# Performance work log

Hardware: AMD Instinct MI355X
Metric: run time of the kernel (lower is better)

The kernel has to match this reference:

```python
import jax, jax.numpy as jnp
import numpy as np

N = 128   # system size (number of sequential RNN steps)
B = 8192  # batch of samples
H = 128   # hidden units per layer (units=[128,128])
D = 2     # input_dim (spin up/down one-hot)


def setup_inputs() -> dict:
    key = jax.random.key(0)
    ks = jax.random.split(key, 11)
    s = 1.0 / np.sqrt(H)  # torch nn.RNNCell/Linear default U(-1/sqrt(H), 1/sqrt(H))
    bits = jax.random.randint(ks[0], (N, B), 0, D)
    samples = jax.nn.one_hot(bits, D, dtype=jnp.float32)  # (N, B, D) one-hot spins
    u = lambda k, shp: jax.random.uniform(k, shp, jnp.float32, -s, s)
    return {
        "samples": samples,
        "W_ih0": u(ks[1], (H, D)), "b_ih0": u(ks[2], (H,)),
        "W_hh0": u(ks[3], (H, H)), "b_hh0": u(ks[4], (H,)),
        "W_ih1": u(ks[5], (H, H)), "b_ih1": u(ks[6], (H,)),
        "W_hh1": u(ks[7], (H, H)), "b_hh1": u(ks[8], (H,)),
        "W_dense": u(ks[9], (D, H)), "b_dense": u(ks[10], (D,)),
    }


def reference(samples, W_ih0, b_ih0, W_hh0, b_hh0,
              W_ih1, b_ih1, W_hh1, b_hh1, W_dense, b_dense):
    # Faithful jax port of RNN_wavefunction.log_prob:
    # p_t = <softmax(dense(h1_t)), s_t>; returns sum_t log p_t with shape (1, B).
    # For one-hot s_t, log(sum(prob*s_t)) == sum(s_t * log_softmax(logits)) (stable form).
    Bsz = samples.shape[1]
    # input at step t is the sampled spin from step t-1; zeros at t=0
    inputs = jnp.concatenate(
        [jnp.zeros((1, Bsz, D), samples.dtype), samples[:-1]], axis=0)
    h0 = jnp.zeros((Bsz, H), samples.dtype)
    h1 = jnp.zeros((Bsz, H), samples.dtype)

    def step(carry, xs):
        h0, h1 = carry
        x_t, s_t = xs  # x_t: (B, D) prev spin one-hot, s_t: (B, D) current spin
        # nn.RNNCell: h' = tanh(x W_ih^T + b_ih + h W_hh^T + b_hh)
        h0 = jnp.tanh(x_t @ W_ih0.T + b_ih0 + h0 @ W_hh0.T + b_hh0)
        h1 = jnp.tanh(h0 @ W_ih1.T + b_ih1 + h1 @ W_hh1.T + b_hh1)
        logits = h1 @ W_dense.T + b_dense           # (B, 2)
        logp = jax.nn.log_softmax(logits, axis=-1)
        lp_t = jnp.sum(logp * s_t, axis=-1)          # (B,) = log p(s_t)
        return (h0, h1), lp_t

    _, lps = jax.lax.scan(step, (h0, h1), (inputs, samples))  # lps: (N, B)
    return jnp.sum(lps, axis=0, keepdims=True)  # (1, B), matches torch keepdim=True
```

## Files before the change

### kernel.cpp

```cpp
#include <hip/hip_runtime.h>
#include <hip/hip_bf16.h>


#define NSTEP 128
#define BTOT  8192
#define HID   128
#define MB    16
#define NBLK  (BTOT / MB)
#define NTHR  512

typedef __attribute__((ext_vector_type(8))) short bf16x8;
typedef __attribute__((ext_vector_type(4))) float f32x4;
typedef __attribute__((ext_vector_type(2))) float f32x2;
typedef __attribute__((ext_vector_type(2))) unsigned uint32x2;

__device__ __forceinline__ short f2bf(float v) {
    unsigned u = __builtin_bit_cast(unsigned, v);
    u += 0x7FFFu + ((u >> 16) & 1u);
    return (short)(u >> 16);
}
__device__ __forceinline__ unsigned cvt2bf(float a, float b) {
    __hip_bfloat162 h2 = __float22bfloat162_rn(make_float2(a, b));
    unsigned u; __builtin_memcpy(&u, &h2, sizeof(u));
    return u;
}
__device__ __forceinline__ f32x2 tanh2(f32x2 x) {
    f32x2 z = x * 2.885390081777927f;
    float e0 = __builtin_exp2f(z.x);
    float e1 = __builtin_exp2f(z.y);
    f32x2 d = {e0 + 1.0f, e1 + 1.0f};
    float r = __builtin_amdgcn_rcpf(d.x * d.y);
    f32x2 inv = {r * d.y, r * d.x};
    return inv * -2.0f + 1.0f;
}

__global__ __launch_bounds__(NTHR, 4) void rnn_wf_kernel(
    const float* __restrict__ samples,
    const float* __restrict__ Wih0,
    const float* __restrict__ bih0,
    const float* __restrict__ Whh0,
    const float* __restrict__ bhh0,
    const float* __restrict__ Wih1,
    const float* __restrict__ bih1,
    const float* __restrict__ Whh1,
    const float* __restrict__ bhh1,
    const float* __restrict__ Wd,
    const float* __restrict__ bd,
    float* __restrict__ out)
{
    __shared__ short sH0[2][MB * HID];
    __shared__ short sH1[2][MB * HID];
    __shared__ unsigned sMask[NSTEP];
    __shared__ float sLd[NSTEP * 17];
    __shared__ __attribute__((aligned(16))) float sBias[4 * HID];
    __shared__ __attribute__((aligned(16))) short sFwd[4 * 64 * 8];

    const int tid  = threadIdx.x;
    const int b0   = blockIdx.x * MB;
    const int w    = tid >> 6;
    const int lane = tid & 63;
    const int q    = lane >> 4;
    const int c    = lane & 15;

    if (tid < NSTEP) {
        unsigned msk = 0;
        #pragma unroll
        for (int m = 0; m < MB; ++m) {
            float e1 = samples[((size_t)tid * BTOT + b0 + m) * 2 + 1];
            if (e1 > 0.5f) msk |= (1u << m);
        }
        sMask[tid] = msk;
    }
    if (tid >= NSTEP && tid < NSTEP + HID) {
        const int n = tid - NSTEP;
        const float bb = bih0[n] + bhh0[n];
        sBias[n]       = bb + Wih0[n * 2 + 0];
        sBias[128 + n] = bb + Wih0[n * 2 + 1];
        sBias[256 + n] = bih1[n] + bhh1[n];
        sBias[384 + n] = bb;
    }
    if (tid >= 256 && tid < 512) {
        const int t2 = tid - 256;
        const int kb = t2 >> 6, l = t2 & 63, cc = l & 15, qq = l >> 4;
        bf16x8 v;
        #pragma unroll
        for (int j = 0; j < 8; ++j)
            v[j] = (cc < 2) ? f2bf(Wd[cc * HID + kb * 32 + qq * 8 + j]) : (short)0;
        *reinterpret_cast<bf16x8*>(&sFwd[(kb * 64 + l) * 8]) = v;
    }

    bf16x8 fhh0[4], fih1[4], fhh1[4];
    {
        const int nn = w * 16 + c;
        #pragma unroll
        for (int kb = 0; kb < 4; ++kb) {
            const int off = nn * HID + kb * 32 + q * 8;
            bf16x8 v0, v1, v2;
            #pragma unroll
            for (int j = 0; j < 8; ++j) {
                v0[j] = f2bf(Whh0[off + j]);
                v1[j] = f2bf(Wih1[off + j]);
                v2[j] = f2bf(Whh1[off + j]);
            }
            fhh0[kb] = v0; fih1[kb] = v1; fhh1[kb] = v2;
        }
    }
    const float bd0 = bd[0], bd1 = bd[1];

    int ra[4];
    #pragma unroll
    for (int kb = 0; kb < 4; ++kb)
        ra[kb] = c * HID + (((kb * 4 + q) ^ c) << 3);
    const int wa = c * HID + (((2 * w + (q >> 1)) ^ c) << 3) + ((q & 1) << 2);
    const int ib = w * 16 + q * 4;

    bool bmPrev = false;

    auto storeL = [&](short* buf, const f32x4& a) {
        f32x2 t0 = tanh2((f32x2){a[0], a[1]});
        f32x2 t1 = tanh2((f32x2){a[2], a[3]});
        uint32x2 v = {cvt2bf(t0.x, t0.y), cvt2bf(t1.x, t1.y)};
        *reinterpret_cast<uint32x2*>(&buf[wa]) = v;
    };

    __syncthreads();

    storeL(sH0[1], *reinterpret_cast<const f32x4*>(&sBias[384 + ib]));
    __syncthreads();

    {
        const bool bmIn = (sMask[0] >> c) & 1u;
        const float* bp = bmIn ? (sBias + 128) : sBias;
        f32x4 a0 = *reinterpret_cast<const f32x4*>(&bp[ib]);
        f32x4 a1 = *reinterpret_cast<const f32x4*>(&sBias[256 + ib]);
        #pragma unroll
        for (int kb = 0; kb < 4; ++kb) {
            bf16x8 f0 = *reinterpret_cast<const bf16x8*>(&sH0[1][ra[kb]]);
            a0 = __builtin_amdgcn_mfma_f32_16x16x32_bf16(fhh0[kb], f0, a0, 0, 0, 0);
            a1 = __builtin_amdgcn_mfma_f32_16x16x32_bf16(fih1[kb], f0, a1, 0, 0, 0);
        }
        storeL(sH0[0], a0);
        storeL(sH1[0], a1);
        bmPrev = bmIn;
        __syncthreads();
    }

    auto stepMain = [&](int i, const short* r0, const short* r1,
                        short* w0b, short* w1b) {
        const bool bmIn = (sMask[i - 1] >> c) & 1u;
        const float* bp = bmIn ? (sBias + 128) : sBias;
        f32x4 a0 = *reinterpret_cast<const f32x4*>(&bp[ib]);
        f32x4 a1 = *reinterpret_cast<const f32x4*>(&sBias[256 + ib]);
        bf16x8 f0[4], f1[4];
        #pragma unroll
        for (int kb = 0; kb < 4; ++kb) {
            f0[kb] = *reinterpret_cast<const bf16x8*>(&r0[ra[kb]]);
            f1[kb] = *reinterpret_cast<const bf16x8*>(&r1[ra[kb]]);
        }
        #pragma unroll
        for (int kb = 0; kb < 4; ++kb) {
            a0 = __builtin_amdgcn_mfma_f32_16x16x32_bf16(fhh0[kb], f0[kb], a0, 0, 0, 0);
            a1 = __builtin_amdgcn_mfma_f32_16x16x32_bf16(fhh1[kb], f1[kb], a1, 0, 0, 0);
        }
        #pragma unroll
        for (int kb = 0; kb < 4; ++kb)
            a1 = __builtin_amdgcn_mfma_f32_16x16x32_bf16(fih1[kb], f0[kb], a1, 0, 0, 0);
        if (w == (i & 7)) {
            f32x4 aL = {bd0, bd1, 0.f, 0.f};
            #pragma unroll
            for (int kb = 0; kb < 4; ++kb) {
                bf16x8 fw = *reinterpret_cast<const bf16x8*>(&sFwd[(kb * 64 + lane) * 8]);
                aL = __builtin_amdgcn_mfma_f32_16x16x32_bf16(fw, f1[kb], aL, 0, 0, 0);
            }
            if (q == 0)
                sLd[(i - 2) * 17 + c] = bmPrev ? (aL[0] - aL[1]) : (aL[1] - aL[0]);
        }
        bmPrev = bmIn;
        storeL(w0b, a0);
        storeL(w1b, a1);
        __syncthreads();
    };

    for (int i = 2; i < NSTEP; i += 2) {
        stepMain(i,     sH0[0], sH1[0], sH0[1], sH1[1]);
        stepMain(i + 1, sH0[1], sH1[1], sH0[0], sH1[0]);
    }

    {
        f32x4 a1 = *reinterpret_cast<const f32x4*>(&sBias[256 + ib]);
        bf16x8 f0[4], f1[4];
        #pragma unroll
        for (int kb = 0; kb < 4; ++kb) {
            f0[kb] = *reinterpret_cast<const bf16x8*>(&sH0[0][ra[kb]]);
            f1[kb] = *reinterpret_cast<const bf16x8*>(&sH1[0][ra[kb]]);
        }
        #pragma unroll
        for (int kb = 0; kb < 4; ++kb)
            a1 = __builtin_amdgcn_mfma_f32_16x16x32_bf16(fhh1[kb], f1[kb], a1, 0, 0, 0);
        #pragma unroll
        for (int kb = 0; kb < 4; ++kb)
            a1 = __builtin_amdgcn_mfma_f32_16x16x32_bf16(fih1[kb], f0[kb], a1, 0, 0, 0);
        if (w == 0) {
            f32x4 aL = {bd0, bd1, 0.f, 0.f};
            #pragma unroll
            for (int kb = 0; kb < 4; ++kb) {
                bf16x8 fw = *reinterpret_cast<const bf16x8*>(&sFwd[(kb * 64 + lane) * 8]);
                aL = __builtin_amdgcn_mfma_f32_16x16x32_bf16(fw, f1[kb], aL, 0, 0, 0);
            }
            if (q == 0)
                sLd[126 * 17 + c] = bmPrev ? (aL[0] - aL[1]) : (aL[1] - aL[0]);
        }
        storeL(sH1[1], a1);
        __syncthreads();
    }
    if (w == 1) {
        f32x4 aL = {bd0, bd1, 0.f, 0.f};
        #pragma unroll
        for (int kb = 0; kb < 4; ++kb) {
            bf16x8 f1 = *reinterpret_cast<const bf16x8*>(&sH1[1][ra[kb]]);
            bf16x8 fw = *reinterpret_cast<const bf16x8*>(&sFwd[(kb * 64 + lane) * 8]);
            aL = __builtin_amdgcn_mfma_f32_16x16x32_bf16(fw, f1, aL, 0, 0, 0);
        }
        if (q == 0) {
            const bool bit = (sMask[NSTEP - 1] >> c) & 1u;
            sLd[127 * 17 + c] = bit ? (aL[0] - aL[1]) : (aL[1] - aL[0]);
        }
    }
    __syncthreads();

    if (tid < 256) {
        const int s = tid >> 4;
        const int k = tid & 15;
        float acc = 0.0f;
        #pragma unroll
        for (int j = 0; j < 8; ++j) {
            const float x = sLd[(j * 16 + k) * 17 + s];
            const float ed = __builtin_exp2f(x * 1.4426950408889634f);
            acc -= 0.6931471805599453f * __builtin_log2f(1.0f + ed);
        }
        #pragma unroll
        for (int off = 1; off < 16; off <<= 1)
            acc += __shfl_xor(acc, off, 64);
        if (k == 0)
            out[b0 + s] = acc;
    }
}

extern "C" void kernel_launch(void* const* d_in, const int* in_sizes, int n_in,
                              void* d_out, int out_size, void* d_ws, size_t ws_size,
                              hipStream_t stream) {
    rnn_wf_kernel<<<NBLK, NTHR, 0, stream>>>(
        (const float*)d_in[0],
        (const float*)d_in[1],
        (const float*)d_in[2],
        (const float*)d_in[3],
        (const float*)d_in[4],
        (const float*)d_in[5],
        (const float*)d_in[6],
        (const float*)d_in[7],
        (const float*)d_in[8],
        (const float*)d_in[9],
        (const float*)d_in[10],
        (float*)d_out);
}
```

Before: 239.3 us.

## Halve block to 4 waves, each computing two output tiles with register-held biases

Each block now runs 256 threads (4 waves) instead of 512, and each wave computes two 16-row tiles of the hidden output per step. The per-step load of LDS data for hidden-state fragments is shared across both tiles. Biases and the dense weight fragments move from shared memory into registers. tanh now uses two reciprocals in place of one shared reciprocal. The change aims to cut redundant LDS fragment reads and make barriers cheaper, at the cost of roughly doubled VGPR use per thread (launch bounds 2) and longer serial MFMA chains per wave.

```diff
diff --git a/kernel.cpp b/kernel.cpp
--- a/kernel.cpp
+++ b/kernel.cpp
@@ -7,7 +7,7 @@
 #define HID   128
 #define MB    16
 #define NBLK  (BTOT / MB)
-#define NTHR  512
+#define NTHR  256
 
 typedef __attribute__((ext_vector_type(8))) short bf16x8;
 typedef __attribute__((ext_vector_type(4))) float f32x4;
@@ -26,15 +26,13 @@
 }
 __device__ __forceinline__ f32x2 tanh2(f32x2 x) {
     f32x2 z = x * 2.885390081777927f;
-    float e0 = __builtin_exp2f(z.x);
-    float e1 = __builtin_exp2f(z.y);
-    f32x2 d = {e0 + 1.0f, e1 + 1.0f};
-    float r = __builtin_amdgcn_rcpf(d.x * d.y);
-    f32x2 inv = {r * d.y, r * d.x};
-    return inv * -2.0f + 1.0f;
-}
-
-__global__ __launch_bounds__(NTHR, 4) void rnn_wf_kernel(
+    float r0 = __builtin_amdgcn_rcpf(__builtin_exp2f(z.x) + 1.0f);
+    float r1 = __builtin_amdgcn_rcpf(__builtin_exp2f(z.y) + 1.0f);
+    f32x2 r = {r0, r1};
+    return r * -2.0f + 1.0f;
+}
+
+__global__ __launch_bounds__(NTHR, 2) void rnn_wf_kernel(
     const float* __restrict__ samples,
     const float* __restrict__ Wih0,
     const float* __restrict__ bih0,
@@ -52,8 +50,6 @@
     __shared__ short sH1[2][MB * HID];
     __shared__ unsigned sMask[NSTEP];
     __shared__ float sLd[NSTEP * 17];
-    __shared__ __attribute__((aligned(16))) float sBias[4 * HID];
-    __shared__ __attribute__((aligned(16))) short sFwd[4 * 64 * 8];
 
     const int tid  = threadIdx.x;
     const int b0   = blockIdx.x * MB;
@@ -71,39 +67,53 @@
         }
         sMask[tid] = msk;
     }
-    if (tid >= NSTEP && tid < NSTEP + HID) {
-        const int n = tid - NSTEP;
-        const float bb = bih0[n] + bhh0[n];
-        sBias[n]       = bb + Wih0[n * 2 + 0];
-        sBias[128 + n] = bb + Wih0[n * 2 + 1];
-        sBias[256 + n] = bih1[n] + bhh1[n];
-        sBias[384 + n] = bb;
-    }
-    if (tid >= 256 && tid < 512) {
-        const int t2 = tid - 256;
-        const int kb = t2 >> 6, l = t2 & 63, cc = l & 15, qq = l >> 4;
-        bf16x8 v;
-        #pragma unroll
-        for (int j = 0; j < 8; ++j)
-            v[j] = (cc < 2) ? f2bf(Wd[cc * HID + kb * 32 + qq * 8 + j]) : (short)0;
-        *reinterpret_cast<bf16x8*>(&sFwd[(kb * 64 + l) * 8]) = v;
-    }
-
-    bf16x8 fhh0[4], fih1[4], fhh1[4];
-    {
-        const int nn = w * 16 + c;
-        #pragma unroll
-        for (int kb = 0; kb < 4; ++kb) {
-            const int off = nn * HID + kb * 32 + q * 8;
-            bf16x8 v0, v1, v2;
-            #pragma unroll
-            for (int j = 0; j < 8; ++j) {
-                v0[j] = f2bf(Whh0[off + j]);
-                v1[j] = f2bf(Wih1[off + j]);
-                v2[j] = f2bf(Whh1[off + j]);
+
+    bf16x8 fhh0[2][4], fih1[2][4], fhh1[2][4], fw[4];
+    {
+        auto ldf = [](const float* p) {
+            f32x4 l0 = *reinterpret_cast<const f32x4*>(p);
+            f32x4 l1 = *reinterpret_cast<const f32x4*>(p + 4);
+            bf16x8 v;
+            v[0]=f2bf(l0[0]); v[1]=f2bf(l0[1]); v[2]=f2bf(l0[2]); v[3]=f2bf(l0[3]);
+            v[4]=f2bf(l1[0]); v[5]=f2bf(l1[1]); v[6]=f2bf(l1[2]); v[7]=f2bf(l1[3]);
+            return v;
+        };
+        #pragma unroll
+        for (int t = 0; t < 2; ++t) {
+            const int nn = w * 32 + t * 16 + c;
+            #pragma unroll
+            for (int kb = 0; kb < 4; ++kb) {
+                const int off = nn * HID + kb * 32 + q * 8;
+                fhh0[t][kb] = ldf(Whh0 + off);
+                fih1[t][kb] = ldf(Wih1 + off);
+                fhh1[t][kb] = ldf(Whh1 + off);
             }
-            fhh0[kb] = v0; fih1[kb] = v1; fhh1[kb] = v2;
-        }
+        }
+        #pragma unroll
+        for (int kb = 0; kb < 4; ++kb) {
+            bf16x8 v;
+            #pragma unroll
+            for (int j = 0; j < 8; ++j)
+                v[j] = (c < 2) ? f2bf(Wd[c * HID + kb * 32 + q * 8 + j]) : (short)0;
+            fw[kb] = v;
+        }
+    }
+
+    f32x4 bWA[2], bWB[2], bB1[2], bP[2];
+    #pragma unroll
+    for (int t = 0; t < 2; ++t) {
+        const int n0 = w * 32 + t * 16 + q * 4;
+        f32x4 vi = *reinterpret_cast<const f32x4*>(&bih0[n0]);
+        f32x4 vh = *reinterpret_cast<const f32x4*>(&bhh0[n0]);
+        f32x4 bb = vi + vh;
+        f32x4 wA = *reinterpret_cast<const f32x4*>(&Wih0[n0 * 2]);
+        f32x4 wB = *reinterpret_cast<const f32x4*>(&Wih0[n0 * 2 + 4]);
+        bP[t]  = bb;
+        bWA[t] = bb + (f32x4){wA[0], wA[2], wB[0], wB[2]};
+        bWB[t] = bb + (f32x4){wA[1], wA[3], wB[1], wB[3]};
+        f32x4 v1 = *reinterpret_cast<const f32x4*>(&bih1[n0]);
+        f32x4 v2 = *reinterpret_cast<const f32x4*>(&bhh1[n0]);
+        bB1[t] = v1 + v2;
     }
     const float bd0 = bd[0], bd1 = bd[1];
 
@@ -111,36 +121,45 @@
     #pragma unroll
     for (int kb = 0; kb < 4; ++kb)
         ra[kb] = c * HID + (((kb * 4 + q) ^ c) << 3);
-    const int wa = c * HID + (((2 * w + (q >> 1)) ^ c) << 3) + ((q & 1) << 2);
-    const int ib = w * 16 + q * 4;
+    int wa[2];
+    #pragma unroll
+    for (int t = 0; t < 2; ++t)
+        wa[t] = c * HID + (((4 * w + 2 * t + (q >> 1)) ^ c) << 3) + ((q & 1) << 2);
 
     bool bmPrev = false;
 
-    auto storeL = [&](short* buf, const f32x4& a) {
+    auto storeT = [&](short* buf, int t, const f32x4& a) {
         f32x2 t0 = tanh2((f32x2){a[0], a[1]});
         f32x2 t1 = tanh2((f32x2){a[2], a[3]});
         uint32x2 v = {cvt2bf(t0.x, t0.y), cvt2bf(t1.x, t1.y)};
-        *reinterpret_cast<uint32x2*>(&buf[wa]) = v;
+        *reinterpret_cast<uint32x2*>(&buf[wa[t]]) = v;
     };
 
     __syncthreads();
 
-    storeL(sH0[1], *reinterpret_cast<const f32x4*>(&sBias[384 + ib]));
+    storeT(sH0[1], 0, bP[0]);
+    storeT(sH0[1], 1, bP[1]);
     __syncthreads();
 
     {
         const bool bmIn = (sMask[0] >> c) & 1u;
-        const float* bp = bmIn ? (sBias + 128) : sBias;
-        f32x4 a0 = *reinterpret_cast<const f32x4*>(&bp[ib]);
-        f32x4 a1 = *reinterpret_cast<const f32x4*>(&sBias[256 + ib]);
-        #pragma unroll
-        for (int kb = 0; kb < 4; ++kb) {
-            bf16x8 f0 = *reinterpret_cast<const bf16x8*>(&sH0[1][ra[kb]]);
-            a0 = __builtin_amdgcn_mfma_f32_16x16x32_bf16(fhh0[kb], f0, a0, 0, 0, 0);
-            a1 = __builtin_amdgcn_mfma_f32_16x16x32_bf16(fih1[kb], f0, a1, 0, 0, 0);
-        }
-        storeL(sH0[0], a0);
-        storeL(sH1[0], a1);
+        bf16x8 f0[4];
+        #pragma unroll
+        for (int kb = 0; kb < 4; ++kb)
+            f0[kb] = *reinterpret_cast<const bf16x8*>(&sH0[1][ra[kb]]);
+        f32x4 a0[2], a1[2];
+        #pragma unroll
+        for (int t = 0; t < 2; ++t) { a0[t] = bmIn ? bWB[t] : bWA[t]; a1[t] = bB1[t]; }
+        #pragma unroll
+        for (int kb = 0; kb < 4; ++kb) {
+            #pragma unroll
+            for (int t = 0; t < 2; ++t) {
+                a0[t] = __builtin_amdgcn_mfma_f32_16x16x32_bf16(fhh0[t][kb], f0[kb], a0[t], 0, 0, 0);
+                a1[t] = __builtin_amdgcn_mfma_f32_16x16x32_bf16(fih1[t][kb], f0[kb], a1[t], 0, 0, 0);
+            }
+        }
+        #pragma unroll
+        for (int t = 0; t < 2; ++t) { storeT(sH0[0], t, a0[t]); storeT(sH1[0], t, a1[t]); }
         bmPrev = bmIn;
         __syncthreads();
     }
@@ -148,36 +167,40 @@
     auto stepMain = [&](int i, const short* r0, const short* r1,
                         short* w0b, short* w1b) {
         const bool bmIn = (sMask[i - 1] >> c) & 1u;
-        const float* bp = bmIn ? (sBias + 128) : sBias;
-        f32x4 a0 = *reinterpret_cast<const f32x4*>(&bp[ib]);
-        f32x4 a1 = *reinterpret_cast<const f32x4*>(&sBias[256 + ib]);
         bf16x8 f0[4], f1[4];
         #pragma unroll
         for (int kb = 0; kb < 4; ++kb) {
             f0[kb] = *reinterpret_cast<const bf16x8*>(&r0[ra[kb]]);
             f1[kb] = *reinterpret_cast<const bf16x8*>(&r1[ra[kb]]);
         }
-        #pragma unroll
-        for (int kb = 0; kb < 4; ++kb) {
-            a0 = __builtin_amdgcn_mfma_f32_16x16x32_bf16(fhh0[kb], f0[kb], a0, 0, 0, 0);
-            a1 = __builtin_amdgcn_mfma_f32_16x16x32_bf16(fhh1[kb], f1[kb], a1, 0, 0, 0);
-        }
-        #pragma unroll
-        for (int kb = 0; kb < 4; ++kb)
-            a1 = __builtin_amdgcn_mfma_f32_16x16x32_bf16(fih1[kb], f0[kb], a1, 0, 0, 0);
-        if (w == (i & 7)) {
+        f32x4 a0[2], a1[2];
+        #pragma unroll
+        for (int t = 0; t < 2; ++t) { a0[t] = bmIn ? bWB[t] : bWA[t]; a1[t] = bB1[t]; }
+        #pragma unroll
+        for (int kb = 0; kb < 4; ++kb) {
+            #pragma unroll
+            for (int t = 0; t < 2; ++t) {
+                a0[t] = __builtin_amdgcn_mfma_f32_16x16x32_bf16(fhh0[t][kb], f0[kb], a0[t], 0, 0, 0);
+                a1[t] = __builtin_amdgcn_mfma_f32_16x16x32_bf16(fhh1[t][kb], f1[kb], a1[t], 0, 0, 0);
+            }
+        }
+        #pragma unroll
+        for (int kb = 0; kb < 4; ++kb) {
+            #pragma unroll
+            for (int t = 0; t < 2; ++t)
+                a1[t] = __builtin_amdgcn_mfma_f32_16x16x32_bf16(fih1[t][kb], f0[kb], a1[t], 0, 0, 0);
+        }
+        if (w == (i & 3)) {
             f32x4 aL = {bd0, bd1, 0.f, 0.f};
             #pragma unroll
-            for (int kb = 0; kb < 4; ++kb) {
-                bf16x8 fw = *reinterpret_cast<const bf16x8*>(&sFwd[(kb * 64 + lane) * 8]);
-                aL = __builtin_amdgcn_mfma_f32_16x16x32_bf16(fw, f1[kb], aL, 0, 0, 0);
-            }
+            for (int kb = 0; kb < 4; ++kb)
+                aL = __builtin_amdgcn_mfma_f32_16x16x32_bf16(fw[kb], f1[kb], aL, 0, 0, 0);
             if (q == 0)
                 sLd[(i - 2) * 17 + c] = bmPrev ? (aL[0] - aL[1]) : (aL[1] - aL[0]);
         }
         bmPrev = bmIn;
-        storeL(w0b, a0);
-        storeL(w1b, a1);
+        #pragma unroll
+        for (int t = 0; t < 2; ++t) { storeT(w0b, t, a0[t]); storeT(w1b, t, a1[t]); }
         __syncthreads();
     };
 
@@ -187,30 +210,37 @@
     }
 
     {
-        f32x4 a1 = *reinterpret_cast<const f32x4*>(&sBias[256 + ib]);
         bf16x8 f0[4], f1[4];
         #pragma unroll
         for (int kb = 0; kb < 4; ++kb) {
             f0[kb] = *reinterpret_cast<const bf16x8*>(&sH0[0][ra[kb]]);
             f1[kb] = *reinterpret_cast<const bf16x8*>(&sH1[0][ra[kb]]);
         }
-        #pragma unroll
-        for (int kb = 0; kb < 4; ++kb)
-            a1 = __builtin_amdgcn_mfma_f32_16x16x32_bf16(fhh1[kb], f1[kb], a1, 0, 0, 0);
-        #pragma unroll
-        for (int kb = 0; kb < 4; ++kb)
-            a1 = __builtin_amdgcn_mfma_f32_16x16x32_bf16(fih1[kb], f0[kb], a1, 0, 0, 0);
+        f32x4 a1[2];
+        #pragma unroll
+        for (int t = 0; t < 2; ++t) a1[t] = bB1[t];
+        #pragma unroll
+        for (int kb = 0; kb < 4; ++kb) {
+            #pragma unroll
+            for (int t = 0; t < 2; ++t)
+                a1[t] = __builtin_amdgcn_mfma_f32_16x16x32_bf16(fhh1[t][kb], f1[kb], a1[t], 0, 0, 0);
+        }
+        #pragma unroll
+        for (int kb = 0; kb < 4; ++kb) {
+            #pragma unroll
+            for (int t = 0; t < 2; ++t)
+                a1[t] = __builtin_amdgcn_mfma_f32_16x16x32_bf16(fih1[t][kb], f0[kb], a1[t], 0, 0, 0);
+        }
         if (w == 0) {
             f32x4 aL = {bd0, bd1, 0.f, 0.f};
             #pragma unroll
-            for (int kb = 0; kb < 4; ++kb) {
-                bf16x8 fw = *reinterpret_cast<const bf16x8*>(&sFwd[(kb * 64 + lane) * 8]);
-                aL = __builtin_amdgcn_mfma_f32_16x16x32_bf16(fw, f1[kb], aL, 0, 0, 0);
-            }
+            for (int kb = 0; kb < 4; ++kb)
+                aL = __builtin_amdgcn_mfma_f32_16x16x32_bf16(fw[kb], f1[kb], aL, 0, 0, 0);
             if (q == 0)
                 sLd[126 * 17 + c] = bmPrev ? (aL[0] - aL[1]) : (aL[1] - aL[0]);
         }
-        storeL(sH1[1], a1);
+        #pragma unroll
+        for (int t = 0; t < 2; ++t) storeT(sH1[1], t, a1[t]);
         __syncthreads();
     }
     if (w == 1) {
@@ -218,8 +248,7 @@
         #pragma unroll
         for (int kb = 0; kb < 4; ++kb) {
             bf16x8 f1 = *reinterpret_cast<const bf16x8*>(&sH1[1][ra[kb]]);
-            bf16x8 fw = *reinterpret_cast<const bf16x8*>(&sFwd[(kb * 64 + lane) * 8]);
-            aL = __builtin_amdgcn_mfma_f32_16x16x32_bf16(fw, f1, aL, 0, 0, 0);
+            aL = __builtin_amdgcn_mfma_f32_16x16x32_bf16(fw[kb], f1, aL, 0, 0, 0);
         }
         if (q == 0) {
             const bool bit = (sMask[NSTEP - 1] >> c) & 1u;
@@ -228,7 +257,7 @@
     }
     __syncthreads();
 
-    if (tid < 256) {
+    {
         const int s = tid >> 4;
         const int k = tid & 15;
         float acc = 0.0f;
```

After: 255.9 us. 6.9% more time.

## Keep biases and spin masks in registers, split MFMA accumulation chains

Applied to the files above, without the earlier changes.

Per-step LDS reads of the spin mask and bias vectors are replaced by registers. Biases are loaded straight from global memory into per-thread f32x4 values, and each thread packs its sample's 128 spin bits into two 64-bit words that are shifted every step. The dependent MFMA chains are also split into two independent accumulators per layer, summed at the end, to shorten the serial MFMA dependency latency. This costs extra VGPRs and a few vector adds per step, and the LDS footprint shrinks.

```diff
diff --git a/kernel.cpp b/kernel.cpp
--- a/kernel.cpp
+++ b/kernel.cpp
@@ -13,6 +13,8 @@
 typedef __attribute__((ext_vector_type(4))) float f32x4;
 typedef __attribute__((ext_vector_type(2))) float f32x2;
 typedef __attribute__((ext_vector_type(2))) unsigned uint32x2;
+typedef __attribute__((ext_vector_type(4))) unsigned uint32x4;
+typedef unsigned long long u64;
 
 __device__ __forceinline__ short f2bf(float v) {
     unsigned u = __builtin_bit_cast(unsigned, v);
@@ -50,10 +52,9 @@
 {
     __shared__ short sH0[2][MB * HID];
     __shared__ short sH1[2][MB * HID];
-    __shared__ unsigned sMask[NSTEP];
     __shared__ float sLd[NSTEP * 17];
-    __shared__ __attribute__((aligned(16))) float sBias[4 * HID];
     __shared__ __attribute__((aligned(16))) short sFwd[4 * 64 * 8];
+    __shared__ __attribute__((aligned(16))) unsigned sWords[16][4];
 
     const int tid  = threadIdx.x;
     const int b0   = blockIdx.x * MB;
@@ -62,22 +63,16 @@
     const int q    = lane >> 4;
     const int c    = lane & 15;
 
-    if (tid < NSTEP) {
-        unsigned msk = 0;
-        #pragma unroll
-        for (int m = 0; m < MB; ++m) {
-            float e1 = samples[((size_t)tid * BTOT + b0 + m) * 2 + 1];
-            if (e1 > 0.5f) msk |= (1u << m);
-        }
-        sMask[tid] = msk;
-    }
-    if (tid >= NSTEP && tid < NSTEP + HID) {
-        const int n = tid - NSTEP;
-        const float bb = bih0[n] + bhh0[n];
-        sBias[n]       = bb + Wih0[n * 2 + 0];
-        sBias[128 + n] = bb + Wih0[n * 2 + 1];
-        sBias[256 + n] = bih1[n] + bhh1[n];
-        sBias[384 + n] = bb;
+    if (tid < 64) {
+        const int j = tid >> 4;
+        const int s = tid & 15;
+        unsigned word = 0;
+        #pragma unroll
+        for (int tt = 0; tt < 32; ++tt) {
+            float e1 = samples[((size_t)(j * 32 + tt) * BTOT + b0 + s) * 2 + 1];
+            if (e1 > 0.5f) word |= (1u << tt);
+        }
+        sWords[s][j] = word;
     }
     if (tid >= 256 && tid < 512) {
         const int t2 = tid - 256;
@@ -107,12 +102,26 @@
     }
     const float bd0 = bd[0], bd1 = bd[1];
 
+    f32x4 bWA, bWB, bB1, bb;
+    {
+        const int n0 = w * 16 + q * 4;
+        f32x4 vi = *reinterpret_cast<const f32x4*>(&bih0[n0]);
+        f32x4 vh = *reinterpret_cast<const f32x4*>(&bhh0[n0]);
+        bb = vi + vh;
+        f32x4 wA = *reinterpret_cast<const f32x4*>(&Wih0[n0 * 2]);
+        f32x4 wB = *reinterpret_cast<const f32x4*>(&Wih0[n0 * 2 + 4]);
+        bWA = bb + (f32x4){wA[0], wA[2], wB[0], wB[2]};
+        bWB = bb + (f32x4){wA[1], wA[3], wB[1], wB[3]};
+        f32x4 v1 = *reinterpret_cast<const f32x4*>(&bih1[n0]);
+        f32x4 v2 = *reinterpret_cast<const f32x4*>(&bhh1[n0]);
+        bB1 = v1 + v2;
+    }
+
     int ra[4];
     #pragma unroll
     for (int kb = 0; kb < 4; ++kb)
         ra[kb] = c * HID + (((kb * 4 + q) ^ c) << 3);
     const int wa = c * HID + (((2 * w + (q >> 1)) ^ c) << 3) + ((q & 1) << 2);
-    const int ib = w * 16 + q * 4;
 
     bool bmPrev = false;
 
@@ -125,14 +134,22 @@
 
     __syncthreads();
 
-    storeL(sH0[1], *reinterpret_cast<const f32x4*>(&sBias[384 + ib]));
+    u64 mlo, mhi;
+    {
+        const uint32x4 mv = *reinterpret_cast<const uint32x4*>(&sWords[c][0]);
+        mlo = (u64)mv[0] | ((u64)mv[1] << 32);
+        mhi = (u64)mv[2] | ((u64)mv[3] << 32);
+    }
+
+    storeL(sH0[1], bb);
     __syncthreads();
 
     {
-        const bool bmIn = (sMask[0] >> c) & 1u;
-        const float* bp = bmIn ? (sBias + 128) : sBias;
-        f32x4 a0 = *reinterpret_cast<const f32x4*>(&bp[ib]);
-        f32x4 a1 = *reinterpret_cast<const f32x4*>(&sBias[256 + ib]);
+        const bool bmIn = (mlo & 1ull) != 0;
+        f32x4 a0, a1;
+        #pragma unroll
+        for (int k = 0; k < 4; ++k) a0[k] = bmIn ? bWB[k] : bWA[k];
+        a1 = bB1;
         #pragma unroll
         for (int kb = 0; kb < 4; ++kb) {
             bf16x8 f0 = *reinterpret_cast<const bf16x8*>(&sH0[1][ra[kb]]);
@@ -145,26 +162,31 @@
         __syncthreads();
     }
 
-    auto stepMain = [&](int i, const short* r0, const short* r1,
+    auto stepMain = [&](int i, bool bmIn, const short* r0, const short* r1,
                         short* w0b, short* w1b) {
-        const bool bmIn = (sMask[i - 1] >> c) & 1u;
-        const float* bp = bmIn ? (sBias + 128) : sBias;
-        f32x4 a0 = *reinterpret_cast<const f32x4*>(&bp[ib]);
-        f32x4 a1 = *reinterpret_cast<const f32x4*>(&sBias[256 + ib]);
+        f32x4 a0a, a0b, a1a, a1b;
+        #pragma unroll
+        for (int k = 0; k < 4; ++k) a0a[k] = bmIn ? bWB[k] : bWA[k];
+        a0b = (f32x4){0.f, 0.f, 0.f, 0.f};
+        a1a = bB1;
+        a1b = (f32x4){0.f, 0.f, 0.f, 0.f};
         bf16x8 f0[4], f1[4];
         #pragma unroll
         for (int kb = 0; kb < 4; ++kb) {
             f0[kb] = *reinterpret_cast<const bf16x8*>(&r0[ra[kb]]);
             f1[kb] = *reinterpret_cast<const bf16x8*>(&r1[ra[kb]]);
         }
-        #pragma unroll
-        for (int kb = 0; kb < 4; ++kb) {
-            a0 = __builtin_amdgcn_mfma_f32_16x16x32_bf16(fhh0[kb], f0[kb], a0, 0, 0, 0);
-            a1 = __builtin_amdgcn_mfma_f32_16x16x32_bf16(fhh1[kb], f1[kb], a1, 0, 0, 0);
-        }
-        #pragma unroll
-        for (int kb = 0; kb < 4; ++kb)
-            a1 = __builtin_amdgcn_mfma_f32_16x16x32_bf16(fih1[kb], f0[kb], a1, 0, 0, 0);
+        a0a = __builtin_amdgcn_mfma_f32_16x16x32_bf16(fhh0[0], f0[0], a0a, 0, 0, 0);
+        a0b = __builtin_amdgcn_mfma_f32_16x16x32_bf16(fhh0[2], f0[2], a0b, 0, 0, 0);
+        a0a = __builtin_amdgcn_mfma_f32_16x16x32_bf16(fhh0[1], f0[1], a0a, 0, 0, 0);
+        a0b = __builtin_amdgcn_mfma_f32_16x16x32_bf16(fhh0[3], f0[3], a0b, 0, 0, 0);
+        #pragma unroll
+        for (int kb = 0; kb < 4; ++kb) {
+            a1a = __builtin_amdgcn_mfma_f32_16x16x32_bf16(fhh1[kb], f1[kb], a1a, 0, 0, 0);
+            a1b = __builtin_amdgcn_mfma_f32_16x16x32_bf16(fih1[kb], f0[kb], a1b, 0, 0, 0);
+        }
+        f32x4 a0 = a0a + a0b;
+        f32x4 a1 = a1a + a1b;
         if (w == (i & 7)) {
             f32x4 aL = {bd0, bd1, 0.f, 0.f};
             #pragma unroll
@@ -181,13 +203,31 @@
         __syncthreads();
     };
 
-    for (int i = 2; i < NSTEP; i += 2) {
-        stepMain(i,     sH0[0], sH1[0], sH0[1], sH1[1]);
-        stepMain(i + 1, sH0[1], sH1[1], sH0[0], sH1[0]);
-    }
-
-    {
-        f32x4 a1 = *reinterpret_cast<const f32x4*>(&sBias[256 + ib]);
+    {
+        u64 run = (mlo >> 1) | (mhi << 63);
+        for (int p = 0; p < 32; ++p) {
+            const int i = 2 + 2 * p;
+            const bool bA = (run & 1ull) != 0;
+            const bool bB = (run & 2ull) != 0;
+            run >>= 2;
+            stepMain(i,     bA, sH0[0], sH1[0], sH0[1], sH1[1]);
+            stepMain(i + 1, bB, sH0[1], sH1[1], sH0[0], sH1[0]);
+        }
+    }
+    {
+        u64 run = mhi >> 1;
+        for (int p = 0; p < 31; ++p) {
+            const int i = 66 + 2 * p;
+            const bool bA = (run & 1ull) != 0;
+            const bool bB = (run & 2ull) != 0;
+            run >>= 2;
+            stepMain(i,     bA, sH0[0], sH1[0], sH0[1], sH1[1]);
+            stepMain(i + 1, bB, sH0[1], sH1[1], sH0[0], sH1[0]);
+        }
+    }
+
+    {
+        f32x4 a1 = bB1;
         bf16x8 f0[4], f1[4];
         #pragma unroll
         for (int kb = 0; kb < 4; ++kb) {
@@ -222,7 +262,7 @@
             aL = __builtin_amdgcn_mfma_f32_16x16x32_bf16(fw, f1, aL, 0, 0, 0);
         }
         if (q == 0) {
-            const bool bit = (sMask[NSTEP - 1] >> c) & 1u;
+            const bool bit = (mhi >> 63) != 0;
             sLd[127 * 17 + c] = bit ? (aL[0] - aL[1]) : (aL[1] - aL[0]);
         }
     }
```

Measured after the change: 268.1 us. 12.0% more time.

## Process two 16-sample tiles per block to interleave independent MFMA chains

Applied to the files above, without the earlier changes.

Each block now handles 32 samples as two independent 16-sample tiles (A and B), issuing their MFMA chains interleaved so the dependent accumulator chains can hide each other's latency within a step. This halves the number of blocks and the count of per-step barriers per sample, and reuses the register-resident weight fragments across both tiles. In exchange it doubles per-thread register pressure for fragments and accumulators, lowers the launch-bounds occupancy hint from 4 to 2, and halves the grid to 256 blocks, which may leave compute units underused.

```diff
diff --git a/kernel.cpp b/kernel.cpp
--- a/kernel.cpp
+++ b/kernel.cpp
@@ -5,8 +5,8 @@
 #define NSTEP 128
 #define BTOT  8192
 #define HID   128
-#define MB    16
-#define NBLK  (BTOT / MB)
+#define SPB   32
+#define NBLK  (BTOT / SPB)
 #define NTHR  512
 
 typedef __attribute__((ext_vector_type(8))) short bf16x8;
@@ -34,7 +34,7 @@
     return inv * -2.0f + 1.0f;
 }
 
-__global__ __launch_bounds__(NTHR, 4) void rnn_wf_kernel(
+__global__ __launch_bounds__(NTHR, 2) void rnn_wf_kernel(
     const float* __restrict__ samples,
     const float* __restrict__ Wih0,
     const float* __restrict__ bih0,
@@ -48,15 +48,17 @@
     const float* __restrict__ bd,
     float* __restrict__ out)
 {
-    __shared__ short sH0[2][MB * HID];
-    __shared__ short sH1[2][MB * HID];
+    __shared__ short sH0A[2][16 * HID];
+    __shared__ short sH1A[2][16 * HID];
+    __shared__ short sH0B[2][16 * HID];
+    __shared__ short sH1B[2][16 * HID];
     __shared__ unsigned sMask[NSTEP];
-    __shared__ float sLd[NSTEP * 17];
+    __shared__ float sLd[2][NSTEP * 17];
     __shared__ __attribute__((aligned(16))) float sBias[4 * HID];
     __shared__ __attribute__((aligned(16))) short sFwd[4 * 64 * 8];
 
     const int tid  = threadIdx.x;
-    const int b0   = blockIdx.x * MB;
+    const int b0   = blockIdx.x * SPB;
     const int w    = tid >> 6;
     const int lane = tid & 63;
     const int q    = lane >> 4;
@@ -65,7 +67,7 @@
     if (tid < NSTEP) {
         unsigned msk = 0;
         #pragma unroll
-        for (int m = 0; m < MB; ++m) {
+        for (int m = 0; m < SPB; ++m) {
             float e1 = samples[((size_t)tid * BTOT + b0 + m) * 2 + 1];
             if (e1 > 0.5f) msk |= (1u << m);
         }
@@ -114,7 +116,7 @@
     const int wa = c * HID + (((2 * w + (q >> 1)) ^ c) << 3) + ((q & 1) << 2);
     const int ib = w * 16 + q * 4;
 
-    bool bmPrev = false;
+    bool bmPrevA = false, bmPrevB = false;
 
     auto storeL = [&](short* buf, const f32x4& a) {
         f32x2 t0 = tanh2((f32x2){a[0], a[1]});
@@ -125,116 +127,191 @@
 
     __syncthreads();
 
-    storeL(sH0[1], *reinterpret_cast<const f32x4*>(&sBias[384 + ib]));
+    {
+        f32x4 bv = *reinterpret_cast<const f32x4*>(&sBias[384 + ib]);
+        storeL(sH0A[1], bv);
+        storeL(sH0B[1], bv);
+    }
     __syncthreads();
 
     {
-        const bool bmIn = (sMask[0] >> c) & 1u;
-        const float* bp = bmIn ? (sBias + 128) : sBias;
-        f32x4 a0 = *reinterpret_cast<const f32x4*>(&bp[ib]);
-        f32x4 a1 = *reinterpret_cast<const f32x4*>(&sBias[256 + ib]);
-        #pragma unroll
-        for (int kb = 0; kb < 4; ++kb) {
-            bf16x8 f0 = *reinterpret_cast<const bf16x8*>(&sH0[1][ra[kb]]);
-            a0 = __builtin_amdgcn_mfma_f32_16x16x32_bf16(fhh0[kb], f0, a0, 0, 0, 0);
-            a1 = __builtin_amdgcn_mfma_f32_16x16x32_bf16(fih1[kb], f0, a1, 0, 0, 0);
-        }
-        storeL(sH0[0], a0);
-        storeL(sH1[0], a1);
-        bmPrev = bmIn;
+        const unsigned msk = sMask[0];
+        const bool bmA = (msk >> c) & 1u;
+        const bool bmB = (msk >> (16 + c)) & 1u;
+        const float* bpA = bmA ? (sBias + 128) : sBias;
+        const float* bpB = bmB ? (sBias + 128) : sBias;
+        f32x4 a0A = *reinterpret_cast<const f32x4*>(&bpA[ib]);
+        f32x4 a0B = *reinterpret_cast<const f32x4*>(&bpB[ib]);
+        f32x4 a1A = *reinterpret_cast<const f32x4*>(&sBias[256 + ib]);
+        f32x4 a1B = a1A;
+        #pragma unroll
+        for (int kb = 0; kb < 4; ++kb) {
+            bf16x8 f0A = *reinterpret_cast<const bf16x8*>(&sH0A[1][ra[kb]]);
+            bf16x8 f0B = *reinterpret_cast<const bf16x8*>(&sH0B[1][ra[kb]]);
+            a0A = __builtin_amdgcn_mfma_f32_16x16x32_bf16(fhh0[kb], f0A, a0A, 0, 0, 0);
+            a0B = __builtin_amdgcn_mfma_f32_16x16x32_bf16(fhh0[kb], f0B, a0B, 0, 0, 0);
+            a1A = __builtin_amdgcn_mfma_f32_16x16x32_bf16(fih1[kb], f0A, a1A, 0, 0, 0);
+            a1B = __builtin_amdgcn_mfma_f32_16x16x32_bf16(fih1[kb], f0B, a1B, 0, 0, 0);
+        }
+        storeL(sH0A[0], a0A);
+        storeL(sH1A[0], a1A);
+        storeL(sH0B[0], a0B);
+        storeL(sH1B[0], a1B);
+        bmPrevA = bmA; bmPrevB = bmB;
         __syncthreads();
     }
 
-    auto stepMain = [&](int i, const short* r0, const short* r1,
-                        short* w0b, short* w1b) {
-        const bool bmIn = (sMask[i - 1] >> c) & 1u;
-        const float* bp = bmIn ? (sBias + 128) : sBias;
-        f32x4 a0 = *reinterpret_cast<const f32x4*>(&bp[ib]);
-        f32x4 a1 = *reinterpret_cast<const f32x4*>(&sBias[256 + ib]);
-        bf16x8 f0[4], f1[4];
-        #pragma unroll
-        for (int kb = 0; kb < 4; ++kb) {
-            f0[kb] = *reinterpret_cast<const bf16x8*>(&r0[ra[kb]]);
-            f1[kb] = *reinterpret_cast<const bf16x8*>(&r1[ra[kb]]);
-        }
-        #pragma unroll
-        for (int kb = 0; kb < 4; ++kb) {
-            a0 = __builtin_amdgcn_mfma_f32_16x16x32_bf16(fhh0[kb], f0[kb], a0, 0, 0, 0);
-            a1 = __builtin_amdgcn_mfma_f32_16x16x32_bf16(fhh1[kb], f1[kb], a1, 0, 0, 0);
-        }
-        #pragma unroll
-        for (int kb = 0; kb < 4; ++kb)
-            a1 = __builtin_amdgcn_mfma_f32_16x16x32_bf16(fih1[kb], f0[kb], a1, 0, 0, 0);
+    auto stepMain = [&](int i,
+                        const short* r0A, const short* r1A, short* w0A, short* w1A,
+                        const short* r0B, const short* r1B, short* w0B, short* w1B) {
+        const unsigned msk = sMask[i - 1];
+        const bool bmA = (msk >> c) & 1u;
+        const bool bmB = (msk >> (16 + c)) & 1u;
+        const float* bpA = bmA ? (sBias + 128) : sBias;
+        const float* bpB = bmB ? (sBias + 128) : sBias;
+        f32x4 a0A = *reinterpret_cast<const f32x4*>(&bpA[ib]);
+        f32x4 a0B = *reinterpret_cast<const f32x4*>(&bpB[ib]);
+        f32x4 a1A = *reinterpret_cast<const f32x4*>(&sBias[256 + ib]);
+        f32x4 a1B = a1A;
+        bf16x8 f0A[4], f1A[4], f0B[4], f1B[4];
+        #pragma unroll
+        for (int kb = 0; kb < 4; ++kb) {
+            f0A[kb] = *reinterpret_cast<const bf16x8*>(&r0A[ra[kb]]);
+            f1A[kb] = *reinterpret_cast<const bf16x8*>(&r1A[ra[kb]]);
+            f0B[kb] = *reinterpret_cast<const bf16x8*>(&r0B[ra[kb]]);
+            f1B[kb] = *reinterpret_cast<const bf16x8*>(&r1B[ra[kb]]);
+        }
+        #pragma unroll
+        for (int kb = 0; kb < 4; ++kb) {
+            a0A = __builtin_amdgcn_mfma_f32_16x16x32_bf16(fhh0[kb], f0A[kb], a0A, 0, 0, 0);
+            a0B = __builtin_amdgcn_mfma_f32_16x16x32_bf16(fhh0[kb], f0B[kb], a0B, 0, 0, 0);
+            a1A = __builtin_amdgcn_mfma_f32_16x16x32_bf16(fhh1[kb], f1A[kb], a1A, 0, 0, 0);
+            a1B = __builtin_amdgcn_mfma_f32_16x16x32_bf16(fhh1[kb], f1B[kb], a1B, 0, 0, 0);
+        }
+        #pragma unroll
+        for (int kb = 0; kb < 4; ++kb) {
+            a1A = __builtin_amdgcn_mfma_f32_16x16x32_bf16(fih1[kb], f0A[kb], a1A, 0, 0, 0);
+            a1B = __builtin_amdgcn_mfma_f32_16x16x32_bf16(fih1[kb], f0B[kb], a1B, 0, 0, 0);
+        }
         if (w == (i & 7)) {
             f32x4 aL = {bd0, bd1, 0.f, 0.f};
             #pragma unroll
             for (int kb = 0; kb < 4; ++kb) {
                 bf16x8 fw = *reinterpret_cast<const bf16x8*>(&sFwd[(kb * 64 + lane) * 8]);
-                aL = __builtin_amdgcn_mfma_f32_16x16x32_bf16(fw, f1[kb], aL, 0, 0, 0);
+                aL = __builtin_amdgcn_mfma_f32_16x16x32_bf16(fw, f1A[kb], aL, 0, 0, 0);
             }
             if (q == 0)
-                sLd[(i - 2) * 17 + c] = bmPrev ? (aL[0] - aL[1]) : (aL[1] - aL[0]);
-        }
-        bmPrev = bmIn;
-        storeL(w0b, a0);
-        storeL(w1b, a1);
+                sLd[0][(i - 2) * 17 + c] = bmPrevA ? (aL[0] - aL[1]) : (aL[1] - aL[0]);
+        }
+        if (w == ((i + 4) & 7)) {
+            f32x4 aL = {bd0, bd1, 0.f, 0.f};
+            #pragma unroll
+            for (int kb = 0; kb < 4; ++kb) {
+                bf16x8 fw = *reinterpret_cast<const bf16x8*>(&sFwd[(kb * 64 + lane) * 8]);
+                aL = __builtin_amdgcn_mfma_f32_16x16x32_bf16(fw, f1B[kb], aL, 0, 0, 0);
+            }
+            if (q == 0)
+                sLd[1][(i - 2) * 17 + c] = bmPrevB ? (aL[0] - aL[1]) : (aL[1] - aL[0]);
+        }
+        bmPrevA = bmA; bmPrevB = bmB;
+        storeL(w0A, a0A);
+        storeL(w1A, a1A);
+        storeL(w0B, a0B);
+        storeL(w1B, a1B);
         __syncthreads();
     };
 
     for (int i = 2; i < NSTEP; i += 2) {
-        stepMain(i,     sH0[0], sH1[0], sH0[1], sH1[1]);
-        stepMain(i + 1, sH0[1], sH1[1], sH0[0], sH1[0]);
-    }
-
-    {
-        f32x4 a1 = *reinterpret_cast<const f32x4*>(&sBias[256 + ib]);
-        bf16x8 f0[4], f1[4];
-        #pragma unroll
-        for (int kb = 0; kb < 4; ++kb) {
-            f0[kb] = *reinterpret_cast<const bf16x8*>(&sH0[0][ra[kb]]);
-            f1[kb] = *reinterpret_cast<const bf16x8*>(&sH1[0][ra[kb]]);
-        }
-        #pragma unroll
-        for (int kb = 0; kb < 4; ++kb)
-            a1 = __builtin_amdgcn_mfma_f32_16x16x32_bf16(fhh1[kb], f1[kb], a1, 0, 0, 0);
-        #pragma unroll
-        for (int kb = 0; kb < 4; ++kb)
-            a1 = __builtin_amdgcn_mfma_f32_16x16x32_bf16(fih1[kb], f0[kb], a1, 0, 0, 0);
+        stepMain(i,
+                 sH0A[0], sH1A[0], sH0A[1], sH1A[1],
+                 sH0B[0], sH1B[0], sH0B[1], sH1B[1]);
+        stepMain(i + 1,
+                 sH0A[1], sH1A[1], sH0A[0], sH1A[0],
+                 sH0B[1], sH1B[1], sH0B[0], sH1B[0]);
+    }
+
+    {
+        f32x4 a1A = *reinterpret_cast<const f32x4*>(&sBias[256 + ib]);
+        f32x4 a1B = a1A;
+        bf16x8 f0A[4], f1A[4], f0B[4], f1B[4];
+        #pragma unroll
+        for (int kb = 0; kb < 4; ++kb) {
+            f0A[kb] = *reinterpret_cast<const bf16x8*>(&sH0A[0][ra[kb]]);
+            f1A[kb] = *reinterpret_cast<const bf16x8*>(&sH1A[0][ra[kb]]);
+            f0B[kb] = *reinterpret_cast<const bf16x8*>(&sH0B[0][ra[kb]]);
+            f1B[kb] = *reinterpret_cast<const bf16x8*>(&sH1B[0][ra[kb]]);
+        }
+        #pragma unroll
+        for (int kb = 0; kb < 4; ++kb) {
+            a1A = __builtin_amdgcn_mfma_f32_16x16x32_bf16(fhh1[kb], f1A[kb], a1A, 0, 0, 0);
+            a1B = __builtin_amdgcn_mfma_f32_16x16x32_bf16(fhh1[kb], f1B[kb], a1B, 0, 0, 0);
+        }
+        #pragma unroll
+        for (int kb = 0; kb < 4; ++kb) {
+            a1A = __builtin_amdgcn_mfma_f32_16x16x32_bf16(fih1[kb], f0A[kb], a1A, 0, 0, 0);
+            a1B = __builtin_amdgcn_mfma_f32_16x16x32_bf16(fih1[kb], f0B[kb], a1B, 0, 0, 0);
+        }
         if (w == 0) {
             f32x4 aL = {bd0, bd1, 0.f, 0.f};
             #pragma unroll
             for (int kb = 0; kb < 4; ++kb) {
                 bf16x8 fw = *reinterpret_cast<const bf16x8*>(&sFwd[(kb * 64 + lane) * 8]);
-                aL = __builtin_amdgcn_mfma_f32_16x16x32_bf16(fw, f1[kb], aL, 0, 0, 0);
+                aL = __builtin_amdgcn_mfma_f32_16x16x32_bf16(fw, f1A[kb], aL, 0, 0, 0);
             }
             if (q == 0)
-                sLd[126 * 17 + c] = bmPrev ? (aL[0] - aL[1]) : (aL[1] - aL[0]);
-        }
-        storeL(sH1[1], a1);
+                sLd[0][126 * 17 + c] = bmPrevA ? (aL[0] - aL[1]) : (aL[1] - aL[0]);
+        }
+        if (w == 4) {
+            f32x4 aL = {bd0, bd1, 0.f, 0.f};
+            #pragma unroll
+            for (int kb = 0; kb < 4; ++kb) {
+                bf16x8 fw = *reinterpret_cast<const bf16x8*>(&sFwd[(kb * 64 + lane) * 8]);
+                aL = __builtin_amdgcn_mfma_f32_16x16x32_bf16(fw, f1B[kb], aL, 0, 0, 0);
+            }
+            if (q == 0)
+                sLd[1][126 * 17 + c] = bmPrevB ? (aL[0] - aL[1]) : (aL[1] - aL[0]);
+        }
+        storeL(sH1A[1], a1A);
+        storeL(sH1B[1], a1B);
         __syncthreads();
     }
     if (w == 1) {
         f32x4 aL = {bd0, bd1, 0.f, 0.f};
         #pragma unroll
         for (int kb = 0; kb < 4; ++kb) {
-            bf16x8 f1 = *reinterpret_cast<const bf16x8*>(&sH1[1][ra[kb]]);
+            bf16x8 f1 = *reinterpret_cast<const bf16x8*>(&sH1A[1][ra[kb]]);
             bf16x8 fw = *reinterpret_cast<const bf16x8*>(&sFwd[(kb * 64 + lane) * 8]);
             aL = __builtin_amdgcn_mfma_f32_16x16x32_bf16(fw, f1, aL, 0, 0, 0);
         }
         if (q == 0) {
             const bool bit = (sMask[NSTEP - 1] >> c) & 1u;
-            sLd[127 * 17 + c] = bit ? (aL[0] - aL[1]) : (aL[1] - aL[0]);
+            sLd[0][127 * 17 + c] = bit ? (aL[0] - aL[1]) : (aL[1] - aL[0]);
+        }
+    }
+    if (w == 5) {
+        f32x4 aL = {bd0, bd1, 0.f, 0.f};
+        #pragma unroll
+        for (int kb = 0; kb < 4; ++kb) {
+            bf16x8 f1 = *reinterpret_cast<const bf16x8*>(&sH1B[1][ra[kb]]);
+            bf16x8 fw = *reinterpret_cast<const bf16x8*>(&sFwd[(kb * 64 + lane) * 8]);
+            aL = __builtin_amdgcn_mfma_f32_16x16x32_bf16(fw, f1, aL, 0, 0, 0);
+        }
+        if (q == 0) {
+            const bool bit = (sMask[NSTEP - 1] >> (16 + c)) & 1u;
+            sLd[1][127 * 17 + c] = bit ? (aL[0] - aL[1]) : (aL[1] - aL[0]);
         }
     }
     __syncthreads();
 
-    if (tid < 256) {
-        const int s = tid >> 4;
-        const int k = tid & 15;
+    {
+        const int s  = tid >> 4;
+        const int k  = tid & 15;
+        const int tb = s >> 4;
+        const int si = s & 15;
         float acc = 0.0f;
         #pragma unroll
         for (int j = 0; j < 8; ++j) {
-            const float x = sLd[(j * 16 + k) * 17 + s];
+            const float x = sLd[tb][(j * 16 + k) * 17 + si];
             const float ed = __builtin_exp2f(x * 1.4426950408889634f);
             acc -= 0.6931471805599453f * __builtin_log2f(1.0f + ed);
         }
```

Measured after the change: 251.5 us. 1.05x slower.
